# Performance work log

Measured on AMD Instinct MI355X. Metric: run time of the kernel, lower is better.

## Reference

```python
import jax, jax.numpy as jnp
import numpy as np

H = 256

def setup_inputs() -> dict:
    key = jax.random.key(0)
    ks = jax.random.split(key, 8)
    B, S = 32, 4096
    hidden = jax.random.normal(ks[0], (B, H), dtype=jnp.float32)
    encoder_outputs = jax.random.normal(ks[1], (B, S, H), dtype=jnp.float32)
    scale = 1.0 / np.sqrt(H)
    W1_w = jax.random.uniform(ks[2], (H, H), jnp.float32, -scale, scale)
    W1_b = jax.random.uniform(ks[3], (H,), jnp.float32, -scale, scale)
    W2_w = jax.random.uniform(ks[4], (H, H), jnp.float32, -scale, scale)
    W2_b = jax.random.uniform(ks[5], (H,), jnp.float32, -scale, scale)
    V_w = jax.random.uniform(ks[6], (H, 1), jnp.float32, -scale, scale)
    V_b = jax.random.uniform(ks[7], (1,), jnp.float32, -scale, scale)
    return {"hidden": hidden, "encoder_outputs": encoder_outputs,
            "W1_w": W1_w, "W1_b": W1_b, "W2_w": W2_w, "W2_b": W2_b,
            "V_w": V_w, "V_b": V_b}

def reference(hidden, encoder_outputs, W1_w, W1_b, W2_w, W2_b, V_w, V_b):
    # hidden: (B,H), encoder_outputs: (B,S,H)
    q = hidden @ W1_w + W1_b                     # (B,H)
    k = jnp.einsum('bsh,hd->bsd', encoder_outputs, W2_w) + W2_b  # (B,S,H)
    energy = jnp.tanh(q[:, None, :] + k)         # (B,S,H)
    scores = jnp.einsum('bsh,ho->bso', energy, V_w) + V_b        # (B,S,1)
    attention_weights = jax.nn.softmax(scores, axis=1)           # (B,S,1)
    context_vector = jnp.einsum('bso,bsh->bh', attention_weights, encoder_outputs)  # (B,H)
    return attention_weights, context_vector
```

## Files before the change

### kernel.cpp

```cpp
#include <hip/hip_runtime.h>
#include <hip/hip_bf16.h>
#include <math.h>

#define BB 32
#define SS 4096
#define HH 256

typedef __bf16 bf16x8 __attribute__((ext_vector_type(8)));
typedef float f32x4 __attribute__((ext_vector_type(4)));

#define GLOBAL_AS __attribute__((address_space(1)))
#define LDS_AS    __attribute__((address_space(3)))

__device__ inline bf16x8 cvt8(const float4& x, const float4& y) {
    union { __hip_bfloat162 p[4]; bf16x8 v; } u;
    u.p[0] = __float22bfloat162_rn(make_float2(x.x, x.y));
    u.p[1] = __float22bfloat162_rn(make_float2(x.z, x.w));
    u.p[2] = __float22bfloat162_rn(make_float2(y.x, y.y));
    u.p[3] = __float22bfloat162_rn(make_float2(y.z, y.w));
    return u.v;
}

__device__ inline float fast_tanh(float x) {
    float e = __builtin_amdgcn_exp2f(x * 2.8853900817779268f);
    return 1.f - 2.f * __builtin_amdgcn_rcpf(e + 1.f);
}

__global__ void prep_kernel(const float* __restrict__ W2_w,
                            ushort* __restrict__ w2sw,
                            const float* __restrict__ hidden,
                            const float* __restrict__ W1_w,
                            const float* __restrict__ W1_b,
                            const float* __restrict__ W2_b,
                            const float* __restrict__ V_w,
                            float* __restrict__ qq,
                            float* __restrict__ Mout) {
    __shared__ float red[HH];
    const int t = threadIdx.x;
    if (blockIdx.x < 256) {
        const int i = blockIdx.x * 256 + t;
        const int j    = i & 7;
        const int lane = (i >> 3) & 63;
        const int nt   = (i >> 9) & 15;
        const int kc   = i >> 13;
        const int k = kc * 32 + ((lane >> 4) & 3) * 8 + j;
        const int n = nt * 16 + (lane & 15);
        __hip_bfloat16 h = __float2bfloat16(W2_w[k * HH + n]);
        w2sw[i] = *(ushort*)&h;
    } else if (blockIdx.x < 256 + BB) {
        const int b = blockIdx.x - 256;
        red[t] = hidden[b * HH + t];
        __syncthreads();
        float acc = 0.f;
#pragma unroll 16
        for (int k = 0; k < HH; ++k)
            acc = fmaf(red[k], W1_w[k * HH + t], acc);
        qq[b * HH + t] = acc + W1_b[t] + W2_b[t];
    } else {
        red[t] = fabsf(V_w[t]);
        __syncthreads();
        for (int off = 128; off > 0; off >>= 1) {
            if (t < off) red[t] += red[t + off];
            __syncthreads();
        }
        if (t == 0) Mout[0] = red[0];
    }
}

__global__ __launch_bounds__(256, 2)
void score_ctx_kernel(const float* __restrict__ enc,
                      const ushort* __restrict__ w2sw,
                      const float* __restrict__ qq,
                      const float* __restrict__ V_w,
                      const float* __restrict__ Mptr,
                      float* __restrict__ wtilde,
                      float* __restrict__ part) {
    extern __shared__ __align__(16) char smem[];
    float* sc_lds = (float*)(smem + 73728);
    float* accl   = (float*)(smem + 49152);

    const int t    = threadIdx.x;
    const int b    = blockIdx.y;
    const int c    = blockIdx.x;
    const int s0   = c * 64;
    const int wave = t >> 6;
    const int lane = t & 63;
    const int mw   = wave & 1;
    const int nw   = wave >> 1;
    const int l15  = lane & 15;
    const int quad = lane >> 4;

    const float* encA = enc + ((size_t)(b * SS + s0)) * HH;
    const int arow = wave * 16 + (lane >> 3);
    const int aswz = 4 * ((lane & 7) ^ (lane >> 3));

#define STAGE(KC, D)                                                          \
    do {                                                                      \
        const char* gw_ = (const char*)w2sw + (KC) * 16384 + t * 16;          \
        char* lw_ = smem + (D) * 16384 + wave * 1024;                         \
        _Pragma("unroll")                                                     \
        for (int i_ = 0; i_ < 4; ++i_)                                        \
            __builtin_amdgcn_global_load_lds(                                 \
                (const GLOBAL_AS void*)(gw_ + i_ * 4096),                     \
                (LDS_AS void*)(lw_ + i_ * 4096), 16, 0, 0);                   \
        _Pragma("unroll")                                                     \
        for (int i_ = 0; i_ < 2; ++i_)                                        \
            __builtin_amdgcn_global_load_lds(                                 \
                (const GLOBAL_AS void*)(encA + (size_t)(arow + i_ * 8) * HH + \
                                        (KC) * 32 + aswz),                    \
                (LDS_AS void*)(smem + 49152 + (D) * 8192 + wave * 2048 +      \
                               i_ * 1024), 16, 0, 0);                         \
    } while (0)

    f32x4 acc[2][8];
#pragma unroll
    for (int mt = 0; mt < 2; ++mt)
#pragma unroll
        for (int nt = 0; nt < 8; ++nt) acc[mt][nt] = (f32x4)0.f;

    STAGE(0, 0);
    STAGE(1, 1);

#pragma unroll
    for (int kc = 0; kc < 8; ++kc) {
        const int cur = kc % 3;
        if (kc < 6) {
            STAGE(kc + 2, (kc + 2) % 3);
            asm volatile("s_waitcnt vmcnt(12)" ::: "memory");
        } else if (kc == 6) {
            asm volatile("s_waitcnt vmcnt(6)" ::: "memory");
        } else {
            asm volatile("s_waitcnt vmcnt(0)" ::: "memory");
        }
        __builtin_amdgcn_s_barrier();

        const ushort* wbuf = (const ushort*)(smem + cur * 16384);
        const float*  abuf = (const float*)(smem + 49152 + cur * 8192);
        const int r0 = mw * 32 + l15;
        const int sx = (l15 & 7) * 4;
        const float4 ax0 = *(const float4*)&abuf[r0 * 32 + ((quad * 8) ^ sx)];
        const float4 ay0 = *(const float4*)&abuf[r0 * 32 + ((quad * 8 + 4) ^ sx)];
        const float4 ax1 = *(const float4*)&abuf[(r0 + 16) * 32 + ((quad * 8) ^ sx)];
        const float4 ay1 = *(const float4*)&abuf[(r0 + 16) * 32 + ((quad * 8 + 4) ^ sx)];
        const bf16x8 af0 = cvt8(ax0, ay0);
        const bf16x8 af1 = cvt8(ax1, ay1);
#pragma unroll
        for (int nt = 0; nt < 8; ++nt) {
            const bf16x8 bfr =
                *(const bf16x8*)&wbuf[((nw * 8 + nt) * 64 + lane) * 8];
            acc[0][nt] = __builtin_amdgcn_mfma_f32_16x16x32_bf16(
                af0, bfr, acc[0][nt], 0, 0, 0);
            acc[1][nt] = __builtin_amdgcn_mfma_f32_16x16x32_bf16(
                af1, bfr, acc[1][nt], 0, 0, 0);
        }
        asm volatile("s_waitcnt lgkmcnt(0)" ::: "memory");
        __builtin_amdgcn_s_barrier();
    }
#undef STAGE

    float p[2][4] = {{0.f, 0.f, 0.f, 0.f}, {0.f, 0.f, 0.f, 0.f}};
#pragma unroll
    for (int nt = 0; nt < 8; ++nt) {
        const int n = nw * 128 + nt * 16 + l15;
        const float qn = qq[b * HH + n];
        const float vn = V_w[n];
#pragma unroll
        for (int mt = 0; mt < 2; ++mt)
#pragma unroll
            for (int r = 0; r < 4; ++r)
                p[mt][r] = fmaf(vn, fast_tanh(qn + acc[mt][nt][r]), p[mt][r]);
    }
#pragma unroll
    for (int off = 1; off < 16; off <<= 1)
#pragma unroll
        for (int mt = 0; mt < 2; ++mt)
#pragma unroll
            for (int r = 0; r < 4; ++r)
                p[mt][r] += __shfl_xor(p[mt][r], off);

    if (nw == 0 && l15 == 0) {
#pragma unroll
        for (int mt = 0; mt < 2; ++mt)
            *(float4*)&sc_lds[mw * 32 + mt * 16 + quad * 4] =
                make_float4(p[mt][0], p[mt][1], p[mt][2], p[mt][3]);
    }
    __syncthreads();
    const float Mv = Mptr[0];
    if (nw == 1 && l15 == 0) {
#pragma unroll
        for (int mt = 0; mt < 2; ++mt) {
            const int row = mw * 32 + mt * 16 + quad * 4;
            float4 h = *(const float4*)&sc_lds[row];
            float4 v = make_float4(__expf(h.x + p[mt][0] - Mv),
                                   __expf(h.y + p[mt][1] - Mv),
                                   __expf(h.z + p[mt][2] - Mv),
                                   __expf(h.w + p[mt][3] - Mv));
            *(float4*)&sc_lds[row] = v;
            *(float4*)&wtilde[b * SS + s0 + row] = v;
        }
    }
    __syncthreads();

    const int tr = t >> 6;
    const int h0 = (t & 63) * 4;
    float4 a = make_float4(0.f, 0.f, 0.f, 0.f);
    const float* ep = enc + ((size_t)(b * SS + s0)) * HH;
#pragma unroll
    for (int jj = 0; jj < 16; ++jj) {
        const int j = jj * 4 + tr;
        const float4 e = *(const float4*)(ep + (size_t)j * HH + h0);
        const float w = sc_lds[j];
        a.x = fmaf(w, e.x, a.x);
        a.y = fmaf(w, e.y, a.y);
        a.z = fmaf(w, e.z, a.z);
        a.w = fmaf(w, e.w, a.w);
    }
    *(float4*)&accl[tr * HH + h0] = a;
    __syncthreads();

    part[((size_t)(b * 64 + c)) * HH + t] =
        accl[0 * HH + t] + accl[1 * HH + t] + accl[2 * HH + t] +
        accl[3 * HH + t];
}

__global__ __launch_bounds__(256)
void finish_kernel(const float* __restrict__ wtilde,
                   const float* __restrict__ part,
                   float* __restrict__ weights_out,
                   float* __restrict__ ctx_out) {
    __shared__ float red[256];
    __shared__ float linv_s;
    const int b = blockIdx.x;
    const int t = threadIdx.x;

    const float4* wt4 = (const float4*)(wtilde + (size_t)b * SS);
    float4 vals[4];
    float l = 0.f;
#pragma unroll
    for (int i = 0; i < 4; ++i) {
        vals[i] = wt4[i * 256 + t];
        l += vals[i].x + vals[i].y + vals[i].z + vals[i].w;
    }
    red[t] = l;
    __syncthreads();
    for (int off = 128; off > 0; off >>= 1) {
        if (t < off) red[t] += red[t + off];
        __syncthreads();
    }
    if (t == 0) linv_s = 1.f / red[0];
    __syncthreads();
    const float linv = linv_s;

    float4* wo4 = (float4*)(weights_out + (size_t)b * SS);
#pragma unroll
    for (int i = 0; i < 4; ++i) {
        const float4 v = vals[i];
        wo4[i * 256 + t] =
            make_float4(v.x * linv, v.y * linv, v.z * linv, v.w * linv);
    }

    float a = 0.f;
#pragma unroll 8
    for (int c = 0; c < 64; ++c)
        a += part[((size_t)(b * 64 + c)) * HH + t];
    ctx_out[b * HH + t] = a * linv;
}

extern "C" void kernel_launch(void* const* d_in, const int* in_sizes, int n_in,
                              void* d_out, int out_size, void* d_ws, size_t ws_size,
                              hipStream_t stream) {
    const float* hidden = (const float*)d_in[0];
    const float* enc    = (const float*)d_in[1];
    const float* W1_w   = (const float*)d_in[2];
    const float* W1_b   = (const float*)d_in[3];
    const float* W2_w   = (const float*)d_in[4];
    const float* W2_b   = (const float*)d_in[5];
    const float* V_w    = (const float*)d_in[6];
    const float* V_b    = (const float*)d_in[7];
    (void)V_b;

    float* out_weights = (float*)d_out;
    float* out_ctx     = (float*)d_out + BB * SS;

    float* ws      = (float*)d_ws;
    float* ws_qq   = ws;
    float* ws_wt   = ws_qq + BB * HH;
    float* ws_part = ws_wt + BB * SS;
    float* ws_M    = ws_part + BB * 64 * HH;
    ushort* ws_w2  = (ushort*)(ws_M + 4);

    static bool attr_done = false;
    if (!attr_done) {
        hipFuncSetAttribute(reinterpret_cast<const void*>(score_ctx_kernel),
                            hipFuncAttributeMaxDynamicSharedMemorySize,
                            73984);
        attr_done = true;
    }

    prep_kernel<<<dim3(256 + BB + 1), dim3(256), 0, stream>>>(
        W2_w, ws_w2, hidden, W1_w, W1_b, W2_b, V_w, ws_qq, ws_M);
    score_ctx_kernel<<<dim3(SS / 64, BB), dim3(256), 73984, stream>>>(
        enc, ws_w2, ws_qq, V_w, ws_M, ws_wt, ws_part);
    finish_kernel<<<dim3(BB), dim3(256), 0, stream>>>(
        ws_wt, ws_part, out_weights, out_ctx);
}
```

Measured before the change: 240.6 us.

## Stage full encoder tile in LDS once and stream W2 fragments from global

The score kernel now loads the whole 64x256 fp32 encoder tile into swizzled LDS in one pass, instead of pipelining 32-column slices through a triple buffer. The context accumulation reuses that LDS copy rather than reading the encoder rows from global memory a second time. The W2 bf16 fragments are read directly from global into registers, double-buffered, which drops the per-step barriers and the W2 LDS staging. The cost is a single up-front load with no overlap against the MFMA work, and higher register pressure from the two 8-fragment weight buffers.

```diff
diff --git a/kernel.cpp b/kernel.cpp
--- a/kernel.cpp
+++ b/kernel.cpp
@@ -76,8 +76,8 @@
                       float* __restrict__ wtilde,
                       float* __restrict__ part) {
     extern __shared__ __align__(16) char smem[];
-    float* sc_lds = (float*)(smem + 73728);
-    float* accl   = (float*)(smem + 49152);
+    float* sc_lds = (float*)(smem + 65536);
+    float* accl   = (float*)(smem + 65792);
 
     const int t    = threadIdx.x;
     const int b    = blockIdx.y;
@@ -91,72 +91,67 @@
     const int quad = lane >> 4;
 
     const float* encA = enc + ((size_t)(b * SS + s0)) * HH;
-    const int arow = wave * 16 + (lane >> 3);
-    const int aswz = 4 * ((lane & 7) ^ (lane >> 3));
-
-#define STAGE(KC, D)                                                          \
+
+    {
+        const int g = lane;
+#pragma unroll
+        for (int i = 0; i < 16; ++i) {
+            const int row = i * 4 + wave;
+            const int srcf = row * HH + 4 * (g ^ (row & 7));
+            __builtin_amdgcn_global_load_lds(
+                (const GLOBAL_AS void*)(encA + srcf),
+                (LDS_AS void*)(smem + i * 4096 + t * 16), 16, 0, 0);
+        }
+    }
+    __syncthreads();
+
+    f32x4 acc[2][8];
+#pragma unroll
+    for (int mt = 0; mt < 2; ++mt)
+#pragma unroll
+        for (int nt = 0; nt < 8; ++nt) acc[mt][nt] = (f32x4)0.f;
+
+    const ushort* w2l = w2sw + (size_t)lane * 8 + (size_t)nw * 8 * 512;
+
+#define LOADW(DST, KC)                                                        \
+    _Pragma("unroll")                                                         \
+    for (int nt_ = 0; nt_ < 8; ++nt_)                                         \
+        DST[nt_] = *(const bf16x8*)(w2l + ((KC) * 16 + nt_) * 512);
+
+    const int r0 = mw * 32 + l15;
+    const int rs = l15 & 7;
+    const char* arow0 = smem + r0 * 1024;
+    const char* arow1 = smem + (r0 + 16) * 1024;
+
+#define COMPUTE(KC, BF)                                                       \
     do {                                                                      \
-        const char* gw_ = (const char*)w2sw + (KC) * 16384 + t * 16;          \
-        char* lw_ = smem + (D) * 16384 + wave * 1024;                         \
+        const int gb_ = (KC) * 128;                                           \
+        const float4 ax0 = *(const float4*)(arow0 + gb_ + (((quad * 2)     ^ rs) * 16)); \
+        const float4 ay0 = *(const float4*)(arow0 + gb_ + (((quad * 2 + 1) ^ rs) * 16)); \
+        const float4 ax1 = *(const float4*)(arow1 + gb_ + (((quad * 2)     ^ rs) * 16)); \
+        const float4 ay1 = *(const float4*)(arow1 + gb_ + (((quad * 2 + 1) ^ rs) * 16)); \
+        const bf16x8 af0 = cvt8(ax0, ay0);                                    \
+        const bf16x8 af1 = cvt8(ax1, ay1);                                    \
         _Pragma("unroll")                                                     \
-        for (int i_ = 0; i_ < 4; ++i_)                                        \
-            __builtin_amdgcn_global_load_lds(                                 \
-                (const GLOBAL_AS void*)(gw_ + i_ * 4096),                     \
-                (LDS_AS void*)(lw_ + i_ * 4096), 16, 0, 0);                   \
-        _Pragma("unroll")                                                     \
-        for (int i_ = 0; i_ < 2; ++i_)                                        \
-            __builtin_amdgcn_global_load_lds(                                 \
-                (const GLOBAL_AS void*)(encA + (size_t)(arow + i_ * 8) * HH + \
-                                        (KC) * 32 + aswz),                    \
-                (LDS_AS void*)(smem + 49152 + (D) * 8192 + wave * 2048 +      \
-                               i_ * 1024), 16, 0, 0);                         \
+        for (int nt_ = 0; nt_ < 8; ++nt_) {                                   \
+            acc[0][nt_] = __builtin_amdgcn_mfma_f32_16x16x32_bf16(            \
+                af0, BF[nt_], acc[0][nt_], 0, 0, 0);                          \
+            acc[1][nt_] = __builtin_amdgcn_mfma_f32_16x16x32_bf16(            \
+                af1, BF[nt_], acc[1][nt_], 0, 0, 0);                          \
+        }                                                                     \
     } while (0)
 
-    f32x4 acc[2][8];
-#pragma unroll
-    for (int mt = 0; mt < 2; ++mt)
-#pragma unroll
-        for (int nt = 0; nt < 8; ++nt) acc[mt][nt] = (f32x4)0.f;
-
-    STAGE(0, 0);
-    STAGE(1, 1);
-
-#pragma unroll
-    for (int kc = 0; kc < 8; ++kc) {
-        const int cur = kc % 3;
-        if (kc < 6) {
-            STAGE(kc + 2, (kc + 2) % 3);
-            asm volatile("s_waitcnt vmcnt(12)" ::: "memory");
-        } else if (kc == 6) {
-            asm volatile("s_waitcnt vmcnt(6)" ::: "memory");
-        } else {
-            asm volatile("s_waitcnt vmcnt(0)" ::: "memory");
-        }
-        __builtin_amdgcn_s_barrier();
-
-        const ushort* wbuf = (const ushort*)(smem + cur * 16384);
-        const float*  abuf = (const float*)(smem + 49152 + cur * 8192);
-        const int r0 = mw * 32 + l15;
-        const int sx = (l15 & 7) * 4;
-        const float4 ax0 = *(const float4*)&abuf[r0 * 32 + ((quad * 8) ^ sx)];
-        const float4 ay0 = *(const float4*)&abuf[r0 * 32 + ((quad * 8 + 4) ^ sx)];
-        const float4 ax1 = *(const float4*)&abuf[(r0 + 16) * 32 + ((quad * 8) ^ sx)];
-        const float4 ay1 = *(const float4*)&abuf[(r0 + 16) * 32 + ((quad * 8 + 4) ^ sx)];
-        const bf16x8 af0 = cvt8(ax0, ay0);
-        const bf16x8 af1 = cvt8(ax1, ay1);
-#pragma unroll
-        for (int nt = 0; nt < 8; ++nt) {
-            const bf16x8 bfr =
-                *(const bf16x8*)&wbuf[((nw * 8 + nt) * 64 + lane) * 8];
-            acc[0][nt] = __builtin_amdgcn_mfma_f32_16x16x32_bf16(
-                af0, bfr, acc[0][nt], 0, 0, 0);
-            acc[1][nt] = __builtin_amdgcn_mfma_f32_16x16x32_bf16(
-                af1, bfr, acc[1][nt], 0, 0, 0);
-        }
-        asm volatile("s_waitcnt lgkmcnt(0)" ::: "memory");
-        __builtin_amdgcn_s_barrier();
-    }
-#undef STAGE
+    bf16x8 bA[8], bB[8];
+    LOADW(bA, 0);
+#pragma unroll 1
+    for (int kc = 0; kc < 8; kc += 2) {
+        LOADW(bB, kc + 1);
+        COMPUTE(kc, bA);
+        if (kc < 6) LOADW(bA, kc + 2);
+        COMPUTE(kc + 1, bB);
+    }
+#undef LOADW
+#undef COMPUTE
 
     float p[2][4] = {{0.f, 0.f, 0.f, 0.f}, {0.f, 0.f, 0.f, 0.f}};
 #pragma unroll
@@ -201,21 +196,23 @@
     }
     __syncthreads();
 
-    const int tr = t >> 6;
-    const int h0 = (t & 63) * 4;
-    float4 a = make_float4(0.f, 0.f, 0.f, 0.f);
-    const float* ep = enc + ((size_t)(b * SS + s0)) * HH;
-#pragma unroll
-    for (int jj = 0; jj < 16; ++jj) {
-        const int j = jj * 4 + tr;
-        const float4 e = *(const float4*)(ep + (size_t)j * HH + h0);
-        const float w = sc_lds[j];
-        a.x = fmaf(w, e.x, a.x);
-        a.y = fmaf(w, e.y, a.y);
-        a.z = fmaf(w, e.z, a.z);
-        a.w = fmaf(w, e.w, a.w);
-    }
-    *(float4*)&accl[tr * HH + h0] = a;
+    {
+        const int tr = t >> 6;
+        const int g  = t & 63;
+        float4 a = make_float4(0.f, 0.f, 0.f, 0.f);
+#pragma unroll
+        for (int jj = 0; jj < 16; ++jj) {
+            const int j = jj * 4 + tr;
+            const float4 e =
+                *(const float4*)(smem + j * 1024 + ((g ^ (j & 7)) * 16));
+            const float w = sc_lds[j];
+            a.x = fmaf(w, e.x, a.x);
+            a.y = fmaf(w, e.y, a.y);
+            a.z = fmaf(w, e.z, a.z);
+            a.w = fmaf(w, e.w, a.w);
+        }
+        *(float4*)&accl[tr * HH + g * 4] = a;
+    }
     __syncthreads();
 
     part[((size_t)(b * 64 + c)) * HH + t] =
@@ -293,13 +290,13 @@
     if (!attr_done) {
         hipFuncSetAttribute(reinterpret_cast<const void*>(score_ctx_kernel),
                             hipFuncAttributeMaxDynamicSharedMemorySize,
-                            73984);
+                            69888);
         attr_done = true;
     }
 
     prep_kernel<<<dim3(256 + BB + 1), dim3(256), 0, stream>>>(
         W2_w, ws_w2, hidden, W1_w, W1_b, W2_b, V_w, ws_qq, ws_M);
-    score_ctx_kernel<<<dim3(SS / 64, BB), dim3(256), 73984, stream>>>(
+    score_ctx_kernel<<<dim3(SS / 64, BB), dim3(256), 69888, stream>>>(
         enc, ws_w2, ws_qq, V_w, ws_M, ws_wt, ws_part);
     finish_kernel<<<dim3(BB), dim3(256), 0, stream>>>(
         ws_wt, ws_part, out_weights, out_ctx);
```

Result: no change. 237.0 us (-1.5%).
